# Optimization experiments

Measured on AMD Instinct MI355X. Metric: run time of the kernel, lower is better.

## Reference

```python
import jax, jax.numpy as jnp
import numpy as np

B, S, D, H = 2, 2048, 1024, 16
HD = D // H

def setup_inputs() -> dict:
    key = jax.random.key(0)
    ks = jax.random.split(key, 9)
    scale = 1.0 / np.sqrt(D)
    return {
        "query": jax.random.normal(ks[0], (B, S, D), jnp.float32),
        "key":   jax.random.normal(ks[1], (B, S, D), jnp.float32),
        "value": jax.random.normal(ks[2], (B, S, D), jnp.float32),
        "Wq_w": jax.random.normal(ks[3], (D, D), jnp.float32) * scale,
        "Wq_b": jax.random.normal(ks[4], (D,), jnp.float32) * scale,
        "Wk_w": jax.random.normal(ks[5], (D, D), jnp.float32) * scale,
        "Wk_b": jax.random.normal(ks[6], (D,), jnp.float32) * scale,
        "Wv_w": jax.random.normal(ks[7], (D, D), jnp.float32) * scale,
        "Wv_b": jax.random.normal(ks[8], (D,), jnp.float32) * scale,
    }

def reference(query, key, value, Wq_w, Wq_b, Wk_w, Wk_b, Wv_w, Wv_b):
    b, s, d = query.shape
    # torch Linear: y = x @ W.T + b
    Q = query @ Wq_w.T + Wq_b
    K = key   @ Wk_w.T + Wk_b
    V = value @ Wv_w.T + Wv_b
    # [B, H, S, HD]
    Q = Q.reshape(b, -1, H, HD).transpose(0, 2, 1, 3)
    K = K.reshape(b, -1, H, HD).transpose(0, 2, 1, 3)
    V = V.reshape(b, -1, H, HD).transpose(0, 2, 1, 3)
    scores = jnp.einsum("bhqd,bhkd->bhqk", Q, K) / jnp.sqrt(jnp.float32(HD))
    attn = jax.nn.softmax(scores, axis=-1)
    context = jnp.einsum("bhqk,bhkd->bhqd", attn, V)  # [B,H,S,HD]
    attn_output = context.transpose(0, 2, 1, 3).reshape(b, -1, H * HD)  # [B,S,D]
    return (context, attn_output)
```

## Files before the change

kernel.cpp:

```cpp
#include <hip/hip_runtime.h>
#include <hip/hip_bf16.h>

constexpr int Bb = 2, Ss = 2048, Dd = 1024, Hh = 16, HD = 64;
constexpr int Mrows = Bb * Ss;
constexpr float QSCALE = 0.125f * 1.44269504088896f;
constexpr size_t CTX_ELEMS = (size_t)Bb * Hh * Ss * HD;

typedef __attribute__((ext_vector_type(8)))  short        short8;
typedef __attribute__((ext_vector_type(4)))  float        floatx4;
typedef __attribute__((ext_vector_type(16))) float        floatx16;
typedef __attribute__((ext_vector_type(4)))  unsigned int uintx4;
typedef __attribute__((ext_vector_type(8)))  __bf16       bf16x8;

#define DEVI __device__ __forceinline__

DEVI unsigned short f2bf(float f) {
  union { float f; unsigned u; } x; x.f = f;
  return (unsigned short)((x.u + 0x7fffu + ((x.u >> 16) & 1u)) >> 16);
}
DEVI float fexp2(float x) {
#if __has_builtin(__builtin_amdgcn_exp2f)
  return __builtin_amdgcn_exp2f(x);
#else
  return __expf(x * 0.6931471805599453f);
#endif
}

constexpr size_t XE = (size_t)Mrows * Dd;
constexpr size_t WE = (size_t)Dd * Dd;
constexpr size_t OFF_W = 3 * XE;
constexpr size_t OFF_O = 3 * XE + 3 * WE;
constexpr size_t WS_NEED = (OFF_O + 3 * XE) * 2;

__global__ __launch_bounds__(256) void convert_bf16(
    const float* __restrict__ q, const float* __restrict__ k, const float* __restrict__ v,
    const float* __restrict__ wq, const float* __restrict__ wk, const float* __restrict__ wv,
    unsigned short* __restrict__ dst)
{
  const int sel = blockIdx.y;
  const float* src; size_t n, off;
  switch (sel) {
    case 0:  src = q;  n = XE; off = 0;            break;
    case 1:  src = k;  n = XE; off = XE;           break;
    case 2:  src = v;  n = XE; off = 2 * XE;       break;
    case 3:  src = wq; n = WE; off = OFF_W;        break;
    case 4:  src = wk; n = WE; off = OFF_W + WE;   break;
    default: src = wv; n = WE; off = OFF_W + 2*WE; break;
  }
  unsigned short* d = dst + off;
  const size_t stride = (size_t)gridDim.x * blockDim.x;
  for (size_t i = (size_t)blockIdx.x * blockDim.x + threadIdx.x; i < n / 8; i += stride) {
    const floatx4 a = *(const floatx4*)(src + i * 8);
    const floatx4 b = *(const floatx4*)(src + i * 8 + 4);
    short8 o;
    #pragma unroll
    for (int j = 0; j < 4; ++j) { o[j] = (short)f2bf(a[j]); o[4 + j] = (short)f2bf(b[j]); }
    *(short8*)(d + i * 8) = o;
  }
}

template<bool SWAP>
DEVI void store_out(floatx4 (&acc)[4][4], const float* __restrict__ bias,
                    unsigned short* __restrict__ out, float oscale,
                    int bm, int bn, int wm, int wn, int lrow, int lg)
{
  if constexpr (!SWAP) {
    #pragma unroll
    for (int ni = 0; ni < 4; ++ni) {
      const int gcol = bn * 128 + wn + ni * 16 + lrow;
      const float bval = bias[gcol];
      const int h = gcol >> 6, hd = gcol & 63;
      #pragma unroll
      for (int mi = 0; mi < 4; ++mi)
        #pragma unroll
        for (int r = 0; r < 4; ++r) {
          const int grow = bm * 128 + wm + mi * 16 + lg * 4 + r;
          const int b = grow >> 11, s = grow & 2047;
          out[(((size_t)(b * Hh + h) * Ss + s) << 6) + hd] = f2bf((acc[mi][ni][r] + bval) * oscale);
        }
    }
  } else {
    #pragma unroll
    for (int ni = 0; ni < 4; ++ni)
      #pragma unroll
      for (int r = 0; r < 4; ++r) {
        const int n = bn * 128 + wn + ni * 16 + lg * 4 + r;
        const float bval = bias[n];
        #pragma unroll
        for (int mi = 0; mi < 4; ++mi) {
          const int m = bm * 128 + wm + mi * 16 + lrow;
          out[(size_t)n * Mrows + m] = f2bf(acc[mi][ni][r] + bval);
        }
      }
  }
}

DEVI void gload16(const unsigned short* g, unsigned short* l) {
  __builtin_amdgcn_global_load_lds(
      (const __attribute__((address_space(1))) unsigned int*)g,
      (__attribute__((address_space(3))) unsigned int*)l, 16, 0, 0);
}

template<bool SWAP>
DEVI void gemm_core_bf16(const unsigned short* __restrict__ X,
                         const unsigned short* __restrict__ W,
                         const float* __restrict__ bias,
                         unsigned short* __restrict__ out, float oscale,
                         unsigned short* As, unsigned short* Bs, int bm, int bn)
{
  const int t = threadIdx.x, wid = t >> 6, lane = t & 63;
  const int lrow = lane & 15, lg = lane >> 4;
  const int wm = (wid >> 1) * 64, wn = (wid & 1) * 64;

  const int srow = lane >> 3;
  const int gch  = (lane & 7) ^ srow;
  const unsigned short* gA = X + (size_t)(bm * 128 + wid * 32 + srow) * Dd + gch * 8;
  const unsigned short* gB = W + (size_t)(bn * 128 + wid * 32 + srow) * Dd + gch * 8;
  unsigned short* lA = As + wid * 4 * 512;
  unsigned short* lB = Bs + wid * 4 * 512;

  floatx4 acc[4][4];
  #pragma unroll
  for (int i = 0; i < 4; ++i)
    #pragma unroll
    for (int j = 0; j < 4; ++j) acc[i][j] = 0.0f;

  for (int k0 = 0; k0 < Dd; k0 += 64) {
    __syncthreads();
    #pragma unroll
    for (int j = 0; j < 4; ++j) {
      gload16(gA + (size_t)j * 8 * Dd + k0, lA + j * 512);
      gload16(gB + (size_t)j * 8 * Dd + k0, lB + j * 512);
    }
    __syncthreads();

    #pragma unroll
    for (int kf = 0; kf < 2; ++kf) {
      bf16x8 af[4], bf[4];
      #pragma unroll
      for (int mi = 0; mi < 4; ++mi) {
        const int row = wm + mi * 16 + lrow;
        const int ch  = ((kf << 2) | lg) ^ (lrow & 7);
        af[mi] = __builtin_bit_cast(bf16x8, *(const short8*)&As[row * 64 + (ch << 3)]);
      }
      #pragma unroll
      for (int ni = 0; ni < 4; ++ni) {
        const int row = wn + ni * 16 + lrow;
        const int ch  = ((kf << 2) | lg) ^ (lrow & 7);
        bf[ni] = __builtin_bit_cast(bf16x8, *(const short8*)&Bs[row * 64 + (ch << 3)]);
      }
      #pragma unroll
      for (int mi = 0; mi < 4; ++mi)
        #pragma unroll
        for (int ni = 0; ni < 4; ++ni) {
          if constexpr (SWAP)
            acc[mi][ni] = __builtin_amdgcn_mfma_f32_16x16x32_bf16(bf[ni], af[mi], acc[mi][ni], 0, 0, 0);
          else
            acc[mi][ni] = __builtin_amdgcn_mfma_f32_16x16x32_bf16(af[mi], bf[ni], acc[mi][ni], 0, 0, 0);
        }
    }
  }
  store_out<SWAP>(acc, bias, out, oscale, bm, bn, wm, wn, lrow, lg);
}

__global__ __launch_bounds__(256, 3) void qkv_gemm_bf16(
    const unsigned short* __restrict__ ws,
    const float* __restrict__ bq, const float* __restrict__ bk, const float* __restrict__ bv,
    unsigned short* __restrict__ outbase)
{
  __shared__ __align__(16) unsigned short As[128 * 64];
  __shared__ __align__(16) unsigned short Bs[128 * 64];

  const int id  = blockIdx.y * 256 + blockIdx.x;
  const int swz = (id & 7) * 96 + (id >> 3);
  const int sel = swz >> 8;
  const int bx  = swz & 255;
  const int bm = bx >> 3, bn = bx & 7;

  const unsigned short* X = ws + (size_t)sel * XE;
  const unsigned short* W = ws + OFF_W + (size_t)sel * WE;
  const float* bias = sel == 0 ? bq : sel == 1 ? bk : bv;
  unsigned short* out = outbase + (size_t)sel * XE;

  if (sel == 2) gemm_core_bf16<true >(X, W, bias, out, 1.0f,   As, Bs, bm, bn);
  else          gemm_core_bf16<false>(X, W, bias, out, sel == 0 ? QSCALE : 1.0f, As, Bs, bm, bn);
}

constexpr int APAD = 40;

template<bool SWAP>
DEVI void gemm_core_f32(const float* __restrict__ X, const float* __restrict__ W,
                        const float* __restrict__ bias, unsigned short* __restrict__ out,
                        float oscale, unsigned short* As, unsigned short* Bs, int bm, int bn)
{
  const int t = threadIdx.x, wid = t >> 6, lane = t & 63;
  const int lrow = lane & 15, lg = lane >> 4;
  const int wm = (wid >> 1) * 64, wn = (wid & 1) * 64;

  floatx4 acc[4][4];
  #pragma unroll
  for (int i = 0; i < 4; ++i)
    #pragma unroll
    for (int j = 0; j < 4; ++j) acc[i][j] = 0.0f;

  for (int k0 = 0; k0 < Dd; k0 += 32) {
    __syncthreads();
    #pragma unroll
    for (int half = 0; half < 2; ++half) {
      const int cidx = t + half * 256;
      const int r = cidx >> 2, c = cidx & 3;
      {
        const float* ga = X + (size_t)(bm * 128 + r) * Dd + k0 + c * 8;
        const floatx4 x0 = *(const floatx4*)ga;
        const floatx4 x1 = *(const floatx4*)(ga + 4);
        short8 va;
        #pragma unroll
        for (int j = 0; j < 4; ++j) { va[j] = (short)f2bf(x0[j]); va[4+j] = (short)f2bf(x1[j]); }
        *(short8*)&As[r * APAD + c * 8] = va;
      }
      {
        const float* gb = W + (size_t)(bn * 128 + r) * Dd + k0 + c * 8;
        const floatx4 x0 = *(const floatx4*)gb;
        const floatx4 x1 = *(const floatx4*)(gb + 4);
        short8 vb;
        #pragma unroll
        for (int j = 0; j < 4; ++j) { vb[j] = (short)f2bf(x0[j]); vb[4+j] = (short)f2bf(x1[j]); }
        *(short8*)&Bs[r * APAD + c * 8] = vb;
      }
    }
    __syncthreads();

    bf16x8 af[4], bf[4];
    #pragma unroll
    for (int mi = 0; mi < 4; ++mi)
      af[mi] = __builtin_bit_cast(bf16x8, *(const short8*)&As[(wm + mi * 16 + lrow) * APAD + lg * 8]);
    #pragma unroll
    for (int ni = 0; ni < 4; ++ni)
      bf[ni] = __builtin_bit_cast(bf16x8, *(const short8*)&Bs[(wn + ni * 16 + lrow) * APAD + lg * 8]);

    #pragma unroll
    for (int mi = 0; mi < 4; ++mi)
      #pragma unroll
      for (int ni = 0; ni < 4; ++ni) {
        if constexpr (SWAP)
          acc[mi][ni] = __builtin_amdgcn_mfma_f32_16x16x32_bf16(bf[ni], af[mi], acc[mi][ni], 0, 0, 0);
        else
          acc[mi][ni] = __builtin_amdgcn_mfma_f32_16x16x32_bf16(af[mi], bf[ni], acc[mi][ni], 0, 0, 0);
      }
  }
  store_out<SWAP>(acc, bias, out, oscale, bm, bn, wm, wn, lrow, lg);
}

__global__ __launch_bounds__(256, 2) void qkv_gemm_f32(
    const float* __restrict__ q, const float* __restrict__ k, const float* __restrict__ v,
    const float* __restrict__ wq, const float* __restrict__ wk, const float* __restrict__ wv,
    const float* __restrict__ bq, const float* __restrict__ bk, const float* __restrict__ bv,
    unsigned short* __restrict__ outbase)
{
  __shared__ __align__(16) unsigned short As[128 * APAD];
  __shared__ __align__(16) unsigned short Bs[128 * APAD];

  const int id  = blockIdx.y * 256 + blockIdx.x;
  const int swz = (id & 7) * 96 + (id >> 3);
  const int sel = swz >> 8;
  const int bx  = swz & 255;
  const int bm = bx >> 3, bn = bx & 7;

  const float* X = sel == 0 ? q : sel == 1 ? k : v;
  const float* W = sel == 0 ? wq : sel == 1 ? wk : wv;
  const float* bias = sel == 0 ? bq : sel == 1 ? bk : bv;
  unsigned short* out = outbase + (size_t)sel * XE;

  if (sel == 2) gemm_core_f32<true >(X, W, bias, out, 1.0f, As, Bs, bm, bn);
  else          gemm_core_f32<false>(X, W, bias, out, sel == 0 ? QSCALE : 1.0f, As, Bs, bm, bn);
}

__global__ __launch_bounds__(256, 2) void attn_fwd(
    const unsigned short* __restrict__ Qw, const unsigned short* __restrict__ Kw,
    const unsigned short* __restrict__ Vw, float* __restrict__ out)
{
  __shared__ __align__(16) unsigned short Ks[2][64 * 64];
  __shared__ __align__(16) unsigned short Vt[2][64 * 64];

  const int id  = blockIdx.y * 16 + blockIdx.x;
  const int swz = (id & 7) * 64 + (id >> 3);
  const int qb  = swz & 15, bh = swz >> 4;
  const int b   = bh >> 4, h = bh & 15;

  const int t = threadIdx.x, wid = t >> 6, lane = t & 63;
  const int l31 = lane & 31, hi = lane >> 5;
  const unsigned short* Qb = Qw + (size_t)bh * (Ss * HD);
  const unsigned short* Kb = Kw + (size_t)bh * (Ss * HD);
  const unsigned short* Vg = Vw + (size_t)(h * 64) * Mrows + b * Ss;
  const int q0 = qb * 128 + wid * 32;

  bf16x8 qf[4];
  #pragma unroll
  for (int hs = 0; hs < 4; ++hs)
    qf[hs] = __builtin_bit_cast(bf16x8,
        *(const short8*)(Qb + (size_t)(q0 + l31) * 64 + hs * 16 + hi * 8));

  floatx16 ctx[2], lsum;
  #pragma unroll
  for (int nb = 0; nb < 2; ++nb) ctx[nb] = 0.0f;
  lsum = 0.0f;

  short8 ones_s;
  #pragma unroll
  for (int j = 0; j < 8; ++j) ones_s[j] = (short)0x3F80;
  const bf16x8 ones = __builtin_bit_cast(bf16x8, ones_s);

  const int rl = lane >> 3;
  const int cs = (lane & 7) ^ rl;
  auto stage = [&](int kv0, int buf) {
    #pragma unroll
    for (int i = 0; i < 2; ++i) {
      const int row = wid * 16 + i * 8 + rl;
      gload16(Kb + (size_t)(kv0 + row) * 64 + cs * 8, &Ks[buf][(wid * 16 + i * 8) * 64]);
      gload16(Vg + (size_t)row * Mrows + kv0 + cs * 8, &Vt[buf][(wid * 16 + i * 8) * 64]);
    }
  };

  stage(0, 0);

  for (int it = 0; it < Ss / 64; ++it) {
    const int cur = it & 1;
    __syncthreads();
    if (it + 1 < Ss / 64) stage((it + 1) * 64, cur ^ 1);

    floatx16 s[2];
    s[0] = 0.0f; s[1] = 0.0f;
    __builtin_amdgcn_s_setprio(1);
    #pragma unroll
    for (int kvb = 0; kvb < 2; ++kvb)
      #pragma unroll
      for (int hs = 0; hs < 4; ++hs) {
        const int ch = ((hs << 1) | hi) ^ (l31 & 7);
        const bf16x8 kf = __builtin_bit_cast(bf16x8,
            *(const short8*)&Ks[cur][(kvb * 32 + l31) * 64 + (ch << 3)]);
        s[kvb] = __builtin_amdgcn_mfma_f32_32x32x16_bf16(kf, qf[hs], s[kvb], 0, 0, 0);
      }
    __builtin_amdgcn_s_setprio(0);

    #pragma unroll
    for (int kvb = 0; kvb < 2; ++kvb) {
      float p[16];
      #pragma unroll
      for (int r = 0; r < 16; ++r) p[r] = fexp2(s[kvb][r]);
      unsigned int c[8];
      #pragma unroll
      for (int i = 0; i < 8; ++i)
        asm("v_cvt_pk_bf16_f32 %0, %1, %2" : "=v"(c[i]) : "v"(p[2 * i]), "v"(p[2 * i + 1]));

      #pragma unroll
      for (int ks2 = 0; ks2 < 2; ++ks2) {
        unsigned int w0 = c[4 * ks2 + 0], w2 = c[4 * ks2 + 2];
        unsigned int w1 = c[4 * ks2 + 1], w3 = c[4 * ks2 + 3];
        asm("v_permlane32_swap_b32 %0, %1" : "+v"(w0), "+v"(w2));
        asm("v_permlane32_swap_b32 %0, %1" : "+v"(w1), "+v"(w3));
        uintx4 paw; paw[0] = w0; paw[1] = w1; paw[2] = w2; paw[3] = w3;
        const bf16x8 pa = __builtin_bit_cast(bf16x8, paw);

        const int ks = kvb * 2 + ks2;
        __builtin_amdgcn_s_setprio(1);
        lsum = __builtin_amdgcn_mfma_f32_32x32x16_bf16(pa, ones, lsum, 0, 0, 0);
        #pragma unroll
        for (int nb = 0; nb < 2; ++nb) {
          const int ch = ((ks << 1) | hi) ^ (l31 & 7);
          const bf16x8 vf = __builtin_bit_cast(bf16x8,
              *(const short8*)&Vt[cur][(nb * 32 + l31) * 64 + (ch << 3)]);
          ctx[nb] = __builtin_amdgcn_mfma_f32_32x32x16_bf16(pa, vf, ctx[nb], 0, 0, 0);
        }
        __builtin_amdgcn_s_setprio(0);
      }
    }
  }

  #pragma unroll
  for (int r = 0; r < 16; ++r) {
    const float inv = 1.0f / lsum[r];
    const int qrow = q0 + (r & 3) + 8 * (r >> 2) + 4 * hi;
    #pragma unroll
    for (int nb = 0; nb < 2; ++nb) {
      const int hd = nb * 32 + l31;
      const float val = ctx[nb][r] * inv;
      out[((size_t)bh * Ss + qrow) * 64 + hd] = val;
      out[CTX_ELEMS + (((size_t)(b * Ss + qrow)) << 10) + (h << 6) + hd] = val;
    }
  }
}

extern "C" void kernel_launch(void* const* d_in, const int* in_sizes, int n_in,
                              void* d_out, int out_size, void* d_ws, size_t ws_size,
                              hipStream_t stream) {
  const float* q  = (const float*)d_in[0];
  const float* k  = (const float*)d_in[1];
  const float* v  = (const float*)d_in[2];
  const float* wq = (const float*)d_in[3];
  const float* bq = (const float*)d_in[4];
  const float* wk = (const float*)d_in[5];
  const float* bk = (const float*)d_in[6];
  const float* wv = (const float*)d_in[7];
  const float* bv = (const float*)d_in[8];
  unsigned short* ws = (unsigned short*)d_ws;
  float* out = (float*)d_out;

  if (ws_size >= WS_NEED) {
    convert_bf16<<<dim3(256, 6), 256, 0, stream>>>(q, k, v, wq, wk, wv, ws);
    qkv_gemm_bf16<<<dim3(256, 3), 256, 0, stream>>>(ws, bq, bk, bv, ws + OFF_O);
    attn_fwd<<<dim3(16, 32), 256, 0, stream>>>(ws + OFF_O, ws + OFF_O + XE, ws + OFF_O + 2 * XE, out);
  } else {
    qkv_gemm_f32<<<dim3(256, 3), 256, 0, stream>>>(q, k, v, wq, wk, wv, bq, bk, bv, ws);
    attn_fwd<<<dim3(16, 32), 256, 0, stream>>>(ws, ws + XE, ws + 2 * XE, out);
  }
}
```

Measured before the change: 92.97 us.

## Split KV range across two wave groups in attention and reduce via LDS

The attention kernel now launches 512 threads per block. Two groups of four waves each process half of the KV sequence, with separate double-buffered K/V tiles, and their partial context and row sums are merged through shared memory at the end. The row-sum MFMA against a ones vector is replaced by scalar accumulation of exp values plus a permlane swap. This aims to raise parallelism and occupancy for the 512-block grid and cut MFMA work, at the cost of a 64KB LDS footprint and an extra reduction and sync phase.

```diff
diff --git a/kernel.cpp b/kernel.cpp
--- a/kernel.cpp
+++ b/kernel.cpp
@@ -275,20 +275,25 @@
   else          gemm_core_f32<false>(X, W, bias, out, sel == 0 ? QSCALE : 1.0f, As, Bs, bm, bn);
 }
 
-__global__ __launch_bounds__(256, 2) void attn_fwd(
+__global__ __launch_bounds__(512, 4) void attn_fwd8(
     const unsigned short* __restrict__ Qw, const unsigned short* __restrict__ Kw,
     const unsigned short* __restrict__ Vw, float* __restrict__ out)
 {
-  __shared__ __align__(16) unsigned short Ks[2][64 * 64];
-  __shared__ __align__(16) unsigned short Vt[2][64 * 64];
+  __shared__ __align__(16) char smemRaw[65536];
+  unsigned short* KsB = (unsigned short*)smemRaw;
+  unsigned short* VtB = (unsigned short*)(smemRaw + 32768);
+  float* ctxL  = (float*)smemRaw;
+  float* lsumL = (float*)(smemRaw + 32768);
 
   const int id  = blockIdx.y * 16 + blockIdx.x;
   const int swz = (id & 7) * 64 + (id >> 3);
   const int qb  = swz & 15, bh = swz >> 4;
   const int b   = bh >> 4, h = bh & 15;
 
-  const int t = threadIdx.x, wid = t >> 6, lane = t & 63;
+  const int t = threadIdx.x, wid8 = t >> 6, lane = t & 63;
+  const int kh = wid8 >> 2, wid = wid8 & 3;
   const int l31 = lane & 31, hi = lane >> 5;
+  const int kvbase = kh << 10;
   const unsigned short* Qb = Qw + (size_t)bh * (Ss * HD);
   const unsigned short* Kb = Kw + (size_t)bh * (Ss * HD);
   const unsigned short* Vg = Vw + (size_t)(h * 64) * Mrows + b * Ss;
@@ -300,53 +305,49 @@
     qf[hs] = __builtin_bit_cast(bf16x8,
         *(const short8*)(Qb + (size_t)(q0 + l31) * 64 + hs * 16 + hi * 8));
 
-  floatx16 ctx[2], lsum;
-  #pragma unroll
-  for (int nb = 0; nb < 2; ++nb) ctx[nb] = 0.0f;
-  lsum = 0.0f;
-
-  short8 ones_s;
-  #pragma unroll
-  for (int j = 0; j < 8; ++j) ones_s[j] = (short)0x3F80;
-  const bf16x8 ones = __builtin_bit_cast(bf16x8, ones_s);
+  floatx16 ctx[2];
+  ctx[0] = 0.0f; ctx[1] = 0.0f;
+  float lsumv = 0.0f;
 
   const int rl = lane >> 3;
   const int cs = (lane & 7) ^ rl;
-  auto stage = [&](int kv0, int buf) {
+  auto stage = [&](int T) {
+    const int kv0 = kvbase + T * 64;
+    unsigned short* Kd = KsB + (size_t)(kh * 2 + (T & 1)) * 4096;
+    unsigned short* Vd = VtB + (size_t)(kh * 2 + (T & 1)) * 4096;
     #pragma unroll
     for (int i = 0; i < 2; ++i) {
       const int row = wid * 16 + i * 8 + rl;
-      gload16(Kb + (size_t)(kv0 + row) * 64 + cs * 8, &Ks[buf][(wid * 16 + i * 8) * 64]);
-      gload16(Vg + (size_t)row * Mrows + kv0 + cs * 8, &Vt[buf][(wid * 16 + i * 8) * 64]);
+      gload16(Kb + (size_t)(kv0 + row) * 64 + cs * 8, Kd + (wid * 16 + i * 8) * 64);
+      gload16(Vg + (size_t)row * Mrows + kv0 + cs * 8, Vd + (wid * 16 + i * 8) * 64);
     }
   };
 
-  stage(0, 0);
-
-  for (int it = 0; it < Ss / 64; ++it) {
+  stage(0);
+
+  for (int it = 0; it < 16; ++it) {
     const int cur = it & 1;
     __syncthreads();
-    if (it + 1 < Ss / 64) stage((it + 1) * 64, cur ^ 1);
-
-    floatx16 s[2];
-    s[0] = 0.0f; s[1] = 0.0f;
-    __builtin_amdgcn_s_setprio(1);
-    #pragma unroll
-    for (int kvb = 0; kvb < 2; ++kvb)
+    if (it + 1 < 16) stage(it + 1);
+    const unsigned short* Kc = KsB + (size_t)(kh * 2 + cur) * 4096;
+    const unsigned short* Vc = VtB + (size_t)(kh * 2 + cur) * 4096;
+
+    #pragma unroll
+    for (int kvb = 0; kvb < 2; ++kvb) {
+      floatx16 s = 0.0f;
+      __builtin_amdgcn_s_setprio(1);
       #pragma unroll
       for (int hs = 0; hs < 4; ++hs) {
         const int ch = ((hs << 1) | hi) ^ (l31 & 7);
         const bf16x8 kf = __builtin_bit_cast(bf16x8,
-            *(const short8*)&Ks[cur][(kvb * 32 + l31) * 64 + (ch << 3)]);
-        s[kvb] = __builtin_amdgcn_mfma_f32_32x32x16_bf16(kf, qf[hs], s[kvb], 0, 0, 0);
-      }
-    __builtin_amdgcn_s_setprio(0);
-
-    #pragma unroll
-    for (int kvb = 0; kvb < 2; ++kvb) {
+            *(const short8*)&Kc[(kvb * 32 + l31) * 64 + (ch << 3)]);
+        s = __builtin_amdgcn_mfma_f32_32x32x16_bf16(kf, qf[hs], s, 0, 0, 0);
+      }
+      __builtin_amdgcn_s_setprio(0);
+
       float p[16];
       #pragma unroll
-      for (int r = 0; r < 16; ++r) p[r] = fexp2(s[kvb][r]);
+      for (int r = 0; r < 16; ++r) { p[r] = fexp2(s[r]); lsumv += p[r]; }
       unsigned int c[8];
       #pragma unroll
       for (int i = 0; i < 8; ++i)
@@ -363,7 +364,125 @@
 
         const int ks = kvb * 2 + ks2;
         __builtin_amdgcn_s_setprio(1);
-        lsum = __builtin_amdgcn_mfma_f32_32x32x16_bf16(pa, ones, lsum, 0, 0, 0);
+        #pragma unroll
+        for (int nb = 0; nb < 2; ++nb) {
+          const int ch = ((ks << 1) | hi) ^ (l31 & 7);
+          const bf16x8 vf = __builtin_bit_cast(bf16x8,
+              *(const short8*)&Vc[(nb * 32 + l31) * 64 + (ch << 3)]);
+          ctx[nb] = __builtin_amdgcn_mfma_f32_32x32x16_bf16(pa, vf, ctx[nb], 0, 0, 0);
+        }
+        __builtin_amdgcn_s_setprio(0);
+      }
+    }
+  }
+
+  float sa = lsumv, sb = lsumv;
+  asm("v_permlane32_swap_b32 %0, %1" : "+v"(sa), "+v"(sb));
+  const float tot = lsumv + (hi ? sa : sb);
+
+  __syncthreads();
+  if (kh == 1) {
+    #pragma unroll
+    for (int r = 0; r < 16; ++r)
+      #pragma unroll
+      for (int nb = 0; nb < 2; ++nb)
+        ctxL[(nb * 16 + r) * 256 + wid * 64 + lane] = ctx[nb][r];
+    if (hi == 0) lsumL[wid * 32 + l31] = tot;
+  }
+  __syncthreads();
+  if (kh == 0) {
+    if (hi == 0) lsumL[128 + wid * 32 + l31] = tot + lsumL[wid * 32 + l31];
+    #pragma unroll
+    for (int r = 0; r < 16; ++r) {
+      const int wr = (r & 3) + 8 * (r >> 2) + 4 * hi;
+      const float inv = 1.0f / lsumL[128 + wid * 32 + wr];
+      const int qrow = q0 + wr;
+      #pragma unroll
+      for (int nb = 0; nb < 2; ++nb) {
+        const int hd = nb * 32 + l31;
+        const float val = (ctx[nb][r] + ctxL[(nb * 16 + r) * 256 + wid * 64 + lane]) * inv;
+        out[((size_t)bh * Ss + qrow) * 64 + hd] = val;
+        out[CTX_ELEMS + (((size_t)(b * Ss + qrow)) << 10) + (h << 6) + hd] = val;
+      }
+    }
+  }
+}
+
+__global__ __launch_bounds__(256, 4) void attn_fwd_fb(
+    const unsigned short* __restrict__ Qw, const unsigned short* __restrict__ Kw,
+    const unsigned short* __restrict__ Vw, float* __restrict__ out)
+{
+  __shared__ __align__(16) unsigned short Ks[2][64 * 64];
+  __shared__ __align__(16) unsigned short Vt[2][64 * 64];
+  __shared__ float Ld[4][32];
+
+  const int id  = blockIdx.y * 16 + blockIdx.x;
+  const int swz = (id & 7) * 64 + (id >> 3);
+  const int qb  = swz & 15, bh = swz >> 4;
+  const int b   = bh >> 4, h = bh & 15;
+
+  const int t = threadIdx.x, wid = t >> 6, lane = t & 63;
+  const int l31 = lane & 31, hi = lane >> 5;
+  const unsigned short* Qb = Qw + (size_t)bh * (Ss * HD);
+  const unsigned short* Kb = Kw + (size_t)bh * (Ss * HD);
+  const unsigned short* Vg = Vw + (size_t)(h * 64) * Mrows + b * Ss;
+  const int q0 = qb * 128 + wid * 32;
+
+  bf16x8 qf[4];
+  #pragma unroll
+  for (int hs = 0; hs < 4; ++hs)
+    qf[hs] = __builtin_bit_cast(bf16x8,
+        *(const short8*)(Qb + (size_t)(q0 + l31) * 64 + hs * 16 + hi * 8));
+
+  floatx16 ctx[2];
+  ctx[0] = 0.0f; ctx[1] = 0.0f;
+  float lsumv = 0.0f;
+
+  const int rl = lane >> 3;
+  const int cs = (lane & 7) ^ rl;
+  auto stage = [&](int T) {
+    const int kv0 = T * 64, buf = T & 1;
+    #pragma unroll
+    for (int i = 0; i < 2; ++i) {
+      const int row = wid * 16 + i * 8 + rl;
+      gload16(Kb + (size_t)(kv0 + row) * 64 + cs * 8, &Ks[buf][(wid * 16 + i * 8) * 64]);
+      gload16(Vg + (size_t)row * Mrows + kv0 + cs * 8, &Vt[buf][(wid * 16 + i * 8) * 64]);
+    }
+  };
+
+  stage(0);
+
+  for (int it = 0; it < 32; ++it) {
+    const int cur = it & 1;
+    __syncthreads();
+    if (it + 1 < 32) stage(it + 1);
+
+    #pragma unroll
+    for (int kvb = 0; kvb < 2; ++kvb) {
+      floatx16 s = 0.0f;
+      #pragma unroll
+      for (int hs = 0; hs < 4; ++hs) {
+        const int ch = ((hs << 1) | hi) ^ (l31 & 7);
+        const bf16x8 kf = __builtin_bit_cast(bf16x8,
+            *(const short8*)&Ks[cur][(kvb * 32 + l31) * 64 + (ch << 3)]);
+        s = __builtin_amdgcn_mfma_f32_32x32x16_bf16(kf, qf[hs], s, 0, 0, 0);
+      }
+      float p[16];
+      #pragma unroll
+      for (int r = 0; r < 16; ++r) { p[r] = fexp2(s[r]); lsumv += p[r]; }
+      unsigned int c[8];
+      #pragma unroll
+      for (int i = 0; i < 8; ++i)
+        asm("v_cvt_pk_bf16_f32 %0, %1, %2" : "=v"(c[i]) : "v"(p[2 * i]), "v"(p[2 * i + 1]));
+      #pragma unroll
+      for (int ks2 = 0; ks2 < 2; ++ks2) {
+        unsigned int w0 = c[4 * ks2 + 0], w2 = c[4 * ks2 + 2];
+        unsigned int w1 = c[4 * ks2 + 1], w3 = c[4 * ks2 + 3];
+        asm("v_permlane32_swap_b32 %0, %1" : "+v"(w0), "+v"(w2));
+        asm("v_permlane32_swap_b32 %0, %1" : "+v"(w1), "+v"(w3));
+        uintx4 paw; paw[0] = w0; paw[1] = w1; paw[2] = w2; paw[3] = w3;
+        const bf16x8 pa = __builtin_bit_cast(bf16x8, paw);
+        const int ks = kvb * 2 + ks2;
         #pragma unroll
         for (int nb = 0; nb < 2; ++nb) {
           const int ch = ((ks << 1) | hi) ^ (l31 & 7);
@@ -371,15 +490,20 @@
               *(const short8*)&Vt[cur][(nb * 32 + l31) * 64 + (ch << 3)]);
           ctx[nb] = __builtin_amdgcn_mfma_f32_32x32x16_bf16(pa, vf, ctx[nb], 0, 0, 0);
         }
-        __builtin_amdgcn_s_setprio(0);
-      }
-    }
-  }
-
+      }
+    }
+  }
+
+  float sa = lsumv, sb = lsumv;
+  asm("v_permlane32_swap_b32 %0, %1" : "+v"(sa), "+v"(sb));
+  const float tot = lsumv + (hi ? sa : sb);
+
+  if (hi == 0) Ld[wid][l31] = tot;
   #pragma unroll
   for (int r = 0; r < 16; ++r) {
-    const float inv = 1.0f / lsum[r];
-    const int qrow = q0 + (r & 3) + 8 * (r >> 2) + 4 * hi;
+    const int wr = (r & 3) + 8 * (r >> 2) + 4 * hi;
+    const float inv = 1.0f / Ld[wid][wr];
+    const int qrow = q0 + wr;
     #pragma unroll
     for (int nb = 0; nb < 2; ++nb) {
       const int hd = nb * 32 + l31;
@@ -408,9 +532,10 @@
   if (ws_size >= WS_NEED) {
     convert_bf16<<<dim3(256, 6), 256, 0, stream>>>(q, k, v, wq, wk, wv, ws);
     qkv_gemm_bf16<<<dim3(256, 3), 256, 0, stream>>>(ws, bq, bk, bv, ws + OFF_O);
-    attn_fwd<<<dim3(16, 32), 256, 0, stream>>>(ws + OFF_O, ws + OFF_O + XE, ws + OFF_O + 2 * XE, out);
+    attn_fwd8<<<dim3(16, 32), 512, 0, stream>>>(
+        ws + OFF_O, ws + OFF_O + XE, ws + OFF_O + 2 * XE, out);
   } else {
     qkv_gemm_f32<<<dim3(256, 3), 256, 0, stream>>>(q, k, v, wq, wk, wv, bq, bk, bv, ws);
-    attn_fwd<<<dim3(16, 32), 256, 0, stream>>>(ws, ws + XE, ws + 2 * XE, out);
-  }
-}
+    attn_fwd_fb<<<dim3(16, 32), 256, 0, stream>>>(ws, ws + XE, ws + 2 * XE, out);
+  }
+}
```

Result: faster. 88.93 us, median of 2 (-4.3%).
